# Optimization experiments

Hardware: AMD Instinct MI355X
Metric: run time of the kernel (lower is better)

## Reference

```python
import jax, jax.numpy as jnp
import numpy as np

LATENT = 1024
RED = 4            # reduce_proj
GROUPS = 16
K = 3              # kernel_size
PAD = 1
REGIONS = 36
CPG = LATENT // GROUPS   # channels per group (in and out), = 64
NEG = 0.1                # LeakyReLU slope


def l2norm(x, axis=-1):
    # faithful to lavse l2norm: x / sqrt(sum(x^2)) with no eps
    return x / jnp.sqrt(jnp.sum(x * x, axis=axis, keepdims=True))


def leaky(x):
    return jnp.where(x > 0, x, NEG * x)


def setup_inputs() -> dict:
    key = jax.random.key(0)
    ks = jax.random.split(key, 7)
    Bi, Bc, T = 128, 32, 50
    img_embed = jax.random.normal(ks[0], (Bi, REGIONS, LATENT), jnp.float32)
    cap_embed = jax.random.normal(ks[1], (Bc, T, LATENT), jnp.float32)
    lens = jax.random.randint(ks[2], (Bc,), 1, T + 1)  # word counts in [1, T]
    qdim = LATENT // RED
    s1 = 1.0 / np.sqrt(LATENT)
    red_w = jax.random.uniform(ks[3], (LATENT, qdim), jnp.float32, -s1, s1)
    red_b = jax.random.uniform(ks[4], (qdim,), jnp.float32, -s1, s1)
    nw = LATENT * CPG * K  # out_channels * (in_channels // groups) * kernel_size
    s2 = 1.0 / np.sqrt(qdim)
    proj_w = jax.random.uniform(ks[5], (qdim, nw), jnp.float32, -s2, s2)
    proj_b = jax.random.uniform(ks[6], (nw,), jnp.float32, -s2, s2)
    return dict(img_embed=img_embed, cap_embed=cap_embed, lens=lens,
                red_w=red_w, red_b=red_b, proj_w=proj_w, proj_b=proj_b)


def reference(img_embed, cap_embed, lens, red_w, red_b, proj_w, proj_b):
    Bi = img_embed.shape[0]
    Bc, T, C = cap_embed.shape
    # masked mean over the first n_words of each caption -> (Bc, C)
    mask = (jnp.arange(T)[None, :] < lens[:, None]).astype(cap_embed.dtype)
    cap_repr = jnp.sum(cap_embed * mask[:, :, None], axis=1) / lens[:, None].astype(cap_embed.dtype)
    cap_act = leaky(cap_repr)                       # 'cap' gate, (Bc, C)
    # dynamic depthwise-grouped conv weights from reduced query
    q = cap_repr @ red_w + red_b                    # (Bc, qdim)
    w = (q @ proj_w + proj_b).reshape(Bc, LATENT, CPG, K)
    w = jax.nn.softmax(w, axis=-1)                  # weightnorm='softmax' over kernel dim
    w = w.reshape(Bc, GROUPS, CPG, CPG, K)          # (Bc, g, out/g, in/g, K)
    # grouped conv1d over 36 regions, padding=1
    img = img_embed.transpose(0, 2, 1)              # (Bi, C, L)
    imgp = jnp.pad(img, ((0, 0), (0, 0), (PAD, PAD)))
    shif = jnp.stack([imgp[:, :, k:k + REGIONS] for k in range(K)], axis=-1)  # (Bi, C, L, K)
    shif = shif.reshape(Bi, GROUPS, CPG, REGIONS, K)
    out = jnp.einsum('bgilk,ngoik->nbgol', shif, w).reshape(Bc, Bi, LATENT, REGIONS)
    out = leaky(out)
    # (x * cap).mean(-1) == x.mean(-1) * cap since cap broadcasts over positions
    img_vec = l2norm(jnp.mean(out, axis=-1) * cap_act[:, None, :])  # (Bc, Bi, C)
    cap_vec = l2norm(cap_repr)                                      # (Bc, C)
    sims = jnp.einsum('nbc,nc->bn', img_vec, cap_vec)               # (Bi, Bc)
    return sims
```

## Files before the change

kernel.cpp:

```cpp
#include <hip/hip_runtime.h>
#include <math.h>

#define LATENT 1024
#define QDIM 256
#define NW 196608
#define BI 128
#define BC 32
#define TT 50
#define REGIONS 36
#define NGROUPS 16
#define CPG 64
#define NEG 0.1f

typedef __attribute__((ext_vector_type(8))) short short8;
typedef __attribute__((ext_vector_type(16))) float f32x16;

__device__ __forceinline__ float leakyf(float x){ return x > 0.f ? x : NEG * x; }

__device__ __forceinline__ unsigned short f2bf(float x){
    union { float f; unsigned int u; } v; v.f = x;
    unsigned int r = v.u + 0x7FFFu + ((v.u >> 16) & 1u);
    return (unsigned short)(r >> 16);
}

__global__ __launch_bounds__(256) void cap_mean_kernel(
    const float* __restrict__ cap_embed, const int* __restrict__ lens,
    float* __restrict__ cap_repr, float* __restrict__ cap_act,
    float* __restrict__ norm_capr)
{
    const int n = blockIdx.x;
    const int len = lens[n];
    const float invl = 1.f / (float)len;
    const int c4 = threadIdx.x;
    const float* base = cap_embed + (size_t)n * TT * LATENT + c4 * 4;
    float4 s = {0.f, 0.f, 0.f, 0.f};
    for (int t = 0; t < len; ++t) {
        const float4 v = *reinterpret_cast<const float4*>(base + (size_t)t * LATENT);
        s.x += v.x; s.y += v.y; s.z += v.z; s.w += v.w;
    }
    float4 m = {s.x * invl, s.y * invl, s.z * invl, s.w * invl};
    *reinterpret_cast<float4*>(cap_repr + n * LATENT + c4 * 4) = m;
    const float sc = 1.f / 36.f;
    float4 a = {leakyf(m.x) * sc, leakyf(m.y) * sc, leakyf(m.z) * sc, leakyf(m.w) * sc};
    *reinterpret_cast<float4*>(cap_act + n * LATENT + c4 * 4) = a;
    float ss = m.x*m.x + m.y*m.y + m.z*m.z + m.w*m.w;
    #pragma unroll
    for (int off = 32; off; off >>= 1) ss += __shfl_xor(ss, off);
    __shared__ float red4[4];
    if ((threadIdx.x & 63) == 0) red4[threadIdx.x >> 6] = ss;
    __syncthreads();
    if (threadIdx.x == 0) norm_capr[n] = sqrtf(red4[0] + red4[1] + red4[2] + red4[3]);
}

__global__ __launch_bounds__(256) void q_kernel(
    const float* __restrict__ cap_repr, const float* __restrict__ red_w,
    const float* __restrict__ red_b, unsigned short* __restrict__ qbfF)
{
    const int cg = blockIdx.x, n = blockIdx.y;
    const int col = threadIdx.x & 31, ks = threadIdx.x >> 5;
    const float* cr = cap_repr + n * LATENT;
    float p = 0.f;
    const int r0 = ks * 128;
    for (int r = r0; r < r0 + 128; ++r)
        p = fmaf(cr[r], red_w[(size_t)r * QDIM + cg * 32 + col], p);
    __shared__ float part[256];
    part[threadIdx.x] = p;
    __syncthreads();
    if (threadIdx.x < 32) {
        float s = red_b[cg * 32 + col];
        #pragma unroll
        for (int k = 0; k < 8; ++k) s += part[k * 32 + col];
        const int r = cg * 32 + col;
        const int elem = (r >> 4) * 512 + ((r >> 3) & 1) * 256 + n * 8 + (r & 7);
        qbfF[elem] = f2bf(s);
    }
}

__global__ __launch_bounds__(512, 2) void wgen10_kernel(
    const unsigned short* __restrict__ qbfF, const float* __restrict__ proj_w,
    const float* __restrict__ proj_b, unsigned short* __restrict__ Wp2F)
{
    __shared__ float L[768 * 32];
    __shared__ float pbs[768];
    const int tid = threadIdx.x;
    const int bx = blockIdx.x;
    const int colbase = bx * 768;
    const int wv = tid >> 6, lane = tid & 63;
    const int lrow = lane & 31, khalf = lane >> 5;

    for (int i = tid; i < 768; i += 512) pbs[i] = proj_b[colbase + i];

    short8 qfr[16];
    {
        const unsigned short* qp = qbfF + (size_t)lane * 8;
        #pragma unroll
        for (int s = 0; s < 16; ++s)
            qfr[s] = *reinterpret_cast<const short8*>(qp + s * 512);
    }

    const float* pw0 = proj_w + (size_t)(khalf * 8) * NW + colbase + wv * 96 + lrow;
    const float* pw1 = pw0 + 32;
    const float* pw2 = pw0 + 64;

    float a0[8], a1[8], a2[8], b0[8], b1[8], b2[8];
    #pragma unroll
    for (int j = 0; j < 8; ++j) {
        a0[j] = pw0[(size_t)j * NW];
        a1[j] = pw1[(size_t)j * NW];
        a2[j] = pw2[(size_t)j * NW];
    }

    f32x16 acc0 = {}, acc1 = {}, acc2 = {};
    #pragma unroll
    for (int s = 0; s < 16; ++s) {
        if (s < 15) {
            const size_t roff = (size_t)((s + 1) * 16) * NW;
            #pragma unroll
            for (int j = 0; j < 8; ++j) {
                b0[j] = pw0[roff + (size_t)j * NW];
                b1[j] = pw1[roff + (size_t)j * NW];
                b2[j] = pw2[roff + (size_t)j * NW];
            }
        }
        unsigned short u0[8], u1[8], u2[8];
        #pragma unroll
        for (int j = 0; j < 8; ++j) {
            u0[j] = f2bf(a0[j]); u1[j] = f2bf(a1[j]); u2[j] = f2bf(a2[j]);
        }
        acc0 = __builtin_amdgcn_mfma_f32_32x32x16_bf16(*reinterpret_cast<const short8*>(u0), qfr[s], acc0, 0, 0, 0);
        acc1 = __builtin_amdgcn_mfma_f32_32x32x16_bf16(*reinterpret_cast<const short8*>(u1), qfr[s], acc1, 0, 0, 0);
        acc2 = __builtin_amdgcn_mfma_f32_32x32x16_bf16(*reinterpret_cast<const short8*>(u2), qfr[s], acc2, 0, 0, 0);
        #pragma unroll
        for (int j = 0; j < 8; ++j) { a0[j] = b0[j]; a1[j] = b1[j]; a2[j] = b2[j]; }
    }

    __syncthreads();
    #pragma unroll
    for (int reg = 0; reg < 16; ++reg) {
        const int rit = (reg & 3) + 8 * (reg >> 2) + 4 * khalf;
        const int c = wv * 96 + rit;
        L[c * 32 + lrow]        = acc0[reg] + pbs[c];
        L[(c + 32) * 32 + lrow] = acc1[reg] + pbs[c + 32];
        L[(c + 64) * 32 + lrow] = acc2[reg] + pbs[c + 64];
    }
    __syncthreads();

    const int g = bx >> 4;
    const int obase = (bx & 15) * 4;
    for (int idx = tid; idx < 8192; idx += 512) {
        const int n = idx & 31, i = idx >> 5;
        const int c = i * 3;
        const float x0 = L[c * 32 + n], x1 = L[(c+1)*32 + n], x2 = L[(c+2)*32 + n];
        const float m = fmaxf(fmaxf(x0, x1), x2);
        const float e0 = expf(x0 - m), e1 = expf(x1 - m), e2 = expf(x2 - m);
        const float inv = 1.f / (e0 + e1 + e2);
        const int o = obase + (i >> 6);
        const int ii = i & 63;
        const int nt = o >> 5, lrow_o = o & 31;
        const int ks = ii >> 4, kh = (ii >> 3) & 1, j = ii & 7;
        const size_t base = (size_t)(n * 16 + g) * 12288
                          + (size_t)(nt * 4 + ks) * 512
                          + kh * 256 + lrow_o * 8 + j;
        Wp2F[base]        = f2bf(e0 * inv);
        Wp2F[base + 4096] = f2bf(e1 * inv);
        Wp2F[base + 8192] = f2bf(e2 * inv);
    }
}

__global__ __launch_bounds__(576, 3) void conv5_kernel(
    const float* __restrict__ img_embed, const unsigned short* __restrict__ Wp2F,
    const float* __restrict__ cap_repr, const float* __restrict__ cap_act,
    float* __restrict__ part_dot, float* __restrict__ part_ss)
{
    const int g = blockIdx.x, bt = blockIdx.y, nq = blockIdx.z;
    const int b0 = bt * 8;
    __shared__ int4 BsmV[3072];
    char* BsmRaw = (char*)BsmV;
    __shared__ float Sw[2][9][2][64];
    const int tid = threadIdx.x;
    const int wv = tid >> 6, lane = tid & 63;
    const int lrow = lane & 31, khalf = lane >> 5;
    const int ioff = khalf * 16;

    const float* imgG = img_embed + (size_t)b0 * 36 * 1024 + g * 64;
    for (int idx = tid; idx < 2304; idx += 576) {
        const int row_img = idx >> 3, ch = idx & 7;
        const int bbs = row_img / 36;
        const int l = row_img - bbs * 36;
        const float* src = imgG + (size_t)row_img * 1024 + ch * 8;
        const float4 u = *reinterpret_cast<const float4*>(src);
        const float4 v = *reinterpret_cast<const float4*>(src + 4);
        unsigned short r8[8];
        r8[0]=f2bf(u.x); r8[1]=f2bf(u.y); r8[2]=f2bf(u.z); r8[3]=f2bf(u.w);
        r8[4]=f2bf(v.x); r8[5]=f2bf(v.y); r8[6]=f2bf(v.z); r8[7]=f2bf(v.w);
        const int arow = bbs * 38 + l + 1;
        const int byte = (arow * 128 + ch * 16) ^ ((arow & 7) << 4);
        *reinterpret_cast<int4*>(BsmRaw + byte) = *reinterpret_cast<const int4*>(r8);
    }
    if (tid < 128) {
        const int rr = tid >> 3, ch = tid & 7;
        const int arow = (rr >> 1) * 38 + (rr & 1) * 37;
        const int byte = (arow * 128 + ch * 16) ^ ((arow & 7) << 4);
        int4 z; z.x = 0; z.y = 0; z.z = 0; z.w = 0;
        *reinterpret_cast<int4*>(BsmRaw + byte) = z;
    }
    __syncthreads();

    const int rg = wv * 32 + lrow;
    const int bbr = rg / 36;
    const int abase = bbr * 38 + (rg - bbr * 36);
    short8 afr[3][4];
    #pragma unroll
    for (int k = 0; k < 3; ++k)
        #pragma unroll
        for (int ks = 0; ks < 4; ++ks) {
            const int arow = abase + k;
            const int byte = (arow * 128 + ks * 32 + ioff) ^ ((arow & 7) << 4);
            afr[k][ks] = *reinterpret_cast<const short8*>(BsmRaw + byte);
        }
    const int rbase = wv * 32;
    const int bfirst = rbase / 36;
    const int bsplit = (bfirst + 1) * 36 - rbase;
    __syncthreads();

    const int n0 = nq * 16;
    int4 st0, st1, st2;
    {
        const unsigned short* WF = Wp2F + (size_t)(n0 * 16 + g) * 12288;
        st0 = *reinterpret_cast<const int4*>(WF + (size_t)tid * 8);
        st1 = *reinterpret_cast<const int4*>(WF + (size_t)(tid + 576) * 8);
        if (tid < 384) st2 = *reinterpret_cast<const int4*>(WF + (size_t)(tid + 1152) * 8);
        *reinterpret_cast<int4*>(BsmRaw + (size_t)tid * 16) = st0;
        *reinterpret_cast<int4*>(BsmRaw + (size_t)(tid + 576) * 16) = st1;
        if (tid < 384) *reinterpret_cast<int4*>(BsmRaw + (size_t)(tid + 1152) * 16) = st2;
    }
    __syncthreads();

    for (int ni = 0; ni < 16; ++ni) {
        const int n = n0 + ni;
        char* Bcur = BsmRaw + (size_t)(ni & 1) * 24576;
        char* Bnxt = BsmRaw + (size_t)((ni + 1) & 1) * 24576;

        if (ni < 15) {
            const unsigned short* WF = Wp2F + (size_t)((n + 1) * 16 + g) * 12288;
            st0 = *reinterpret_cast<const int4*>(WF + (size_t)tid * 8);
            st1 = *reinterpret_cast<const int4*>(WF + (size_t)(tid + 576) * 8);
            if (tid < 384) st2 = *reinterpret_cast<const int4*>(WF + (size_t)(tid + 1152) * 8);
        }

        f32x16 acc0 = {}, acc1 = {};
        #pragma unroll
        for (int k = 0; k < 3; ++k) {
            #pragma unroll
            for (int ks = 0; ks < 4; ++ks) {
                const char* fb = Bcur + k * 8192 + ks * 1024 + (size_t)lane * 16;
                const short8 bf0 = *reinterpret_cast<const short8*>(fb);
                const short8 bf1 = *reinterpret_cast<const short8*>(fb + 4096);
                acc0 = __builtin_amdgcn_mfma_f32_32x32x16_bf16(afr[k][ks], bf0, acc0, 0, 0, 0);
                acc1 = __builtin_amdgcn_mfma_f32_32x32x16_bf16(afr[k][ks], bf1, acc1, 0, 0, 0);
            }
        }

        if (ni < 15) {
            *reinterpret_cast<int4*>(Bnxt + (size_t)tid * 16) = st0;
            *reinterpret_cast<int4*>(Bnxt + (size_t)(tid + 576) * 16) = st1;
            if (tid < 384) *reinterpret_cast<int4*>(Bnxt + (size_t)(tid + 1152) * 16) = st2;
        }

        float s0A = 0.f, s0B = 0.f, s1A = 0.f, s1B = 0.f;
        #pragma unroll
        for (int reg = 0; reg < 16; ++reg) {
            const int rit = (reg & 3) + 8 * (reg >> 2) + 4 * khalf;
            const float v0 = leakyf(acc0[reg]);
            const float v1 = leakyf(acc1[reg]);
            if (rit >= bsplit) { s0B += v0; s1B += v1; }
            else               { s0A += v0; s1A += v1; }
        }
        s0A += __shfl_xor(s0A, 32); s0B += __shfl_xor(s0B, 32);
        s1A += __shfl_xor(s1A, 32); s1B += __shfl_xor(s1B, 32);
        const int q = ni & 1;
        if (khalf == 0) {
            Sw[q][wv][0][lrow]      = s0A;
            Sw[q][wv][0][32 + lrow] = s1A;
            if (bsplit < 32) {
                Sw[q][wv][1][lrow]      = s0B;
                Sw[q][wv][1][32 + lrow] = s1B;
            }
        }
        __syncthreads();

        if (tid < 128) {
            const int b = tid >> 4, j = tid & 15;
            const float4 ca4 = *reinterpret_cast<const float4*>(&cap_act [n * LATENT + g * CPG + j * 4]);
            const float4 cr4 = *reinterpret_cast<const float4*>(&cap_repr[n * LATENT + g * CPG + j * 4]);
            const float cav[4] = {ca4.x, ca4.y, ca4.z, ca4.w};
            const float crv[4] = {cr4.x, cr4.y, cr4.z, cr4.w};
            float d = 0.f, ss = 0.f;
            #pragma unroll
            for (int u = 0; u < 4; ++u) {
                const int o = j * 4 + u;
                const float S = (b == 0)
                    ? Sw[q][0][0][o] + Sw[q][1][0][o]
                    : Sw[q][b][1][o] + Sw[q][b + 1][0][o];
                const float tmp = S * cav[u];
                d = fmaf(tmp, crv[u], d);
                ss = fmaf(tmp, tmp, ss);
            }
            #pragma unroll
            for (int off = 1; off <= 8; off <<= 1) {
                d += __shfl_xor(d, off);
                ss += __shfl_xor(ss, off);
            }
            if (j == 0) {
                part_dot[((size_t)n * BI + b0 + b) * NGROUPS + g] = d;
                part_ss [((size_t)n * BI + b0 + b) * NGROUPS + g] = ss;
            }
        }
    }
}

__global__ __launch_bounds__(256) void final_kernel(
    const float* __restrict__ part_dot, const float* __restrict__ part_ss,
    const float* __restrict__ norm_capr, float* __restrict__ out)
{
    const int idx = blockIdx.x * 256 + threadIdx.x;
    const int n = idx & 31;
    const int b = idx >> 5;
    const size_t base = ((size_t)n * BI + b) * NGROUPS;
    float d = 0.f, s = 0.f;
    #pragma unroll
    for (int g = 0; g < NGROUPS; ++g) { d += part_dot[base + g]; s += part_ss[base + g]; }
    out[b * BC + n] = d / (sqrtf(s) * norm_capr[n]);
}

extern "C" void kernel_launch(void* const* d_in, const int* in_sizes, int n_in,
                              void* d_out, int out_size, void* d_ws, size_t ws_size,
                              hipStream_t stream) {
    const float* img_embed = (const float*)d_in[0];
    const float* cap_embed = (const float*)d_in[1];
    const int*   lens      = (const int*)  d_in[2];
    const float* red_w     = (const float*)d_in[3];
    const float* red_b     = (const float*)d_in[4];
    const float* proj_w    = (const float*)d_in[5];
    const float* proj_b    = (const float*)d_in[6];
    float* out = (float*)d_out;

    char* ws = (char*)d_ws;
    unsigned short* Wp2F   = (unsigned short*)(ws);
    float* cap_repr  = (float*)(ws + 22020096);
    float* cap_act   = (float*)(ws + 22151168);
    unsigned short* qbfF = (unsigned short*)(ws + 22282240);
    float* norm_capr = (float*)(ws + 22315008);
    float* part_dot  = (float*)(ws + 22315520);
    float* part_ss   = (float*)(ws + 22577664);

    hipLaunchKernelGGL(cap_mean_kernel, dim3(BC), dim3(256), 0, stream,
                       cap_embed, lens, cap_repr, cap_act, norm_capr);
    hipLaunchKernelGGL(q_kernel, dim3(8, BC), dim3(256), 0, stream,
                       cap_repr, red_w, red_b, qbfF);
    hipLaunchKernelGGL(wgen10_kernel, dim3(256), dim3(512), 0, stream,
                       qbfF, proj_w, proj_b, Wp2F);
    hipLaunchKernelGGL(conv5_kernel, dim3(NGROUPS, 16, 2), dim3(576), 0, stream,
                       img_embed, Wp2F, cap_repr, cap_act, part_dot, part_ss);
    hipLaunchKernelGGL(final_kernel, dim3(16), dim3(256), 0, stream,
                       part_dot, part_ss, norm_capr, out);
}
```

Baseline: 176.6 us.

## Double image rows per conv block to reuse each loaded weight tile twice

The conv kernel now handles 16 images per block instead of 8. Each wave computes two 32-row M tiles against the same double-buffered weight tile, and the image tile stays resident in a separate shared buffer. This halves how many times each weight slice is loaded from global memory and reduces the block count. In exchange, shared memory and register pressure rise, since the high tile's A fragments are reloaded from LDS inside the loop. Grid parallelism also halves, from 512 to 256 blocks.

```diff
diff --git a/kernel.cpp b/kernel.cpp
--- a/kernel.cpp
+++ b/kernel.cpp
@@ -167,23 +167,23 @@
     }
 }
 
-__global__ __launch_bounds__(576, 3) void conv5_kernel(
+__global__ __launch_bounds__(576, 3) void conv6_kernel(
     const float* __restrict__ img_embed, const unsigned short* __restrict__ Wp2F,
     const float* __restrict__ cap_repr, const float* __restrict__ cap_act,
     float* __restrict__ part_dot, float* __restrict__ part_ss)
 {
     const int g = blockIdx.x, bt = blockIdx.y, nq = blockIdx.z;
-    const int b0 = bt * 8;
-    __shared__ int4 BsmV[3072];
-    char* BsmRaw = (char*)BsmV;
-    __shared__ float Sw[2][9][2][64];
+    const int b0 = bt * 16;
+    __shared__ char Asm[16 * 38 * 128];
+    __shared__ char Bd[2][24576];
+    __shared__ float Sw[2][18][2][64];
     const int tid = threadIdx.x;
     const int wv = tid >> 6, lane = tid & 63;
     const int lrow = lane & 31, khalf = lane >> 5;
     const int ioff = khalf * 16;
 
     const float* imgG = img_embed + (size_t)b0 * 36 * 1024 + g * 64;
-    for (int idx = tid; idx < 2304; idx += 576) {
+    for (int idx = tid; idx < 4608; idx += 576) {
         const int row_img = idx >> 3, ch = idx & 7;
         const int bbs = row_img / 36;
         const int l = row_img - bbs * 36;
@@ -195,33 +195,40 @@
         r8[4]=f2bf(v.x); r8[5]=f2bf(v.y); r8[6]=f2bf(v.z); r8[7]=f2bf(v.w);
         const int arow = bbs * 38 + l + 1;
         const int byte = (arow * 128 + ch * 16) ^ ((arow & 7) << 4);
-        *reinterpret_cast<int4*>(BsmRaw + byte) = *reinterpret_cast<const int4*>(r8);
-    }
-    if (tid < 128) {
+        *reinterpret_cast<int4*>(Asm + byte) = *reinterpret_cast<const int4*>(r8);
+    }
+    if (tid < 256) {
         const int rr = tid >> 3, ch = tid & 7;
         const int arow = (rr >> 1) * 38 + (rr & 1) * 37;
         const int byte = (arow * 128 + ch * 16) ^ ((arow & 7) << 4);
         int4 z; z.x = 0; z.y = 0; z.z = 0; z.w = 0;
-        *reinterpret_cast<int4*>(BsmRaw + byte) = z;
-    }
-    __syncthreads();
-
-    const int rg = wv * 32 + lrow;
-    const int bbr = rg / 36;
-    const int abase = bbr * 38 + (rg - bbr * 36);
-    short8 afr[3][4];
+        *reinterpret_cast<int4*>(Asm + byte) = z;
+    }
+    __syncthreads();
+
+    const int rlo = wv * 64 + lrow;
+    const int blo = rlo / 36;
+    const int abase_lo = blo * 38 + (rlo - blo * 36);
+    short8 afr[12];
     #pragma unroll
     for (int k = 0; k < 3; ++k)
         #pragma unroll
         for (int ks = 0; ks < 4; ++ks) {
-            const int arow = abase + k;
+            const int arow = abase_lo + k;
             const int byte = (arow * 128 + ks * 32 + ioff) ^ ((arow & 7) << 4);
-            afr[k][ks] = *reinterpret_cast<const short8*>(BsmRaw + byte);
-        }
-    const int rbase = wv * 32;
-    const int bfirst = rbase / 36;
-    const int bsplit = (bfirst + 1) * 36 - rbase;
-    __syncthreads();
+            afr[k * 4 + ks] = *reinterpret_cast<const short8*>(Asm + byte);
+        }
+    const int rhi = wv * 64 + 32 + lrow;
+    const int bhi = rhi / 36;
+    const int abase_hi = bhi * 38 + (rhi - bhi * 36);
+
+    int bfirstT[2], bsplitT[2];
+    #pragma unroll
+    for (int mt = 0; mt < 2; ++mt) {
+        const int rbase = (2 * wv + mt) * 32;
+        bfirstT[mt] = rbase / 36;
+        bsplitT[mt] = (bfirstT[mt] + 1) * 36 - rbase;
+    }
 
     const int n0 = nq * 16;
     int4 st0, st1, st2;
@@ -230,16 +237,16 @@
         st0 = *reinterpret_cast<const int4*>(WF + (size_t)tid * 8);
         st1 = *reinterpret_cast<const int4*>(WF + (size_t)(tid + 576) * 8);
         if (tid < 384) st2 = *reinterpret_cast<const int4*>(WF + (size_t)(tid + 1152) * 8);
-        *reinterpret_cast<int4*>(BsmRaw + (size_t)tid * 16) = st0;
-        *reinterpret_cast<int4*>(BsmRaw + (size_t)(tid + 576) * 16) = st1;
-        if (tid < 384) *reinterpret_cast<int4*>(BsmRaw + (size_t)(tid + 1152) * 16) = st2;
+        *reinterpret_cast<int4*>(Bd[0] + (size_t)tid * 16) = st0;
+        *reinterpret_cast<int4*>(Bd[0] + (size_t)(tid + 576) * 16) = st1;
+        if (tid < 384) *reinterpret_cast<int4*>(Bd[0] + (size_t)(tid + 1152) * 16) = st2;
     }
     __syncthreads();
 
     for (int ni = 0; ni < 16; ++ni) {
         const int n = n0 + ni;
-        char* Bcur = BsmRaw + (size_t)(ni & 1) * 24576;
-        char* Bnxt = BsmRaw + (size_t)((ni + 1) & 1) * 24576;
+        char* Bcur = Bd[ni & 1];
+        char* Bnxt = Bd[(ni + 1) & 1];
 
         if (ni < 15) {
             const unsigned short* WF = Wp2F + (size_t)((n + 1) * 16 + g) * 12288;
@@ -248,7 +255,7 @@
             if (tid < 384) st2 = *reinterpret_cast<const int4*>(WF + (size_t)(tid + 1152) * 8);
         }
 
-        f32x16 acc0 = {}, acc1 = {};
+        f32x16 acc[2][2] = {};
         #pragma unroll
         for (int k = 0; k < 3; ++k) {
             #pragma unroll
@@ -256,8 +263,14 @@
                 const char* fb = Bcur + k * 8192 + ks * 1024 + (size_t)lane * 16;
                 const short8 bf0 = *reinterpret_cast<const short8*>(fb);
                 const short8 bf1 = *reinterpret_cast<const short8*>(fb + 4096);
-                acc0 = __builtin_amdgcn_mfma_f32_32x32x16_bf16(afr[k][ks], bf0, acc0, 0, 0, 0);
-                acc1 = __builtin_amdgcn_mfma_f32_32x32x16_bf16(afr[k][ks], bf1, acc1, 0, 0, 0);
+                const int arh = abase_hi + k;
+                const int byteH = (arh * 128 + ks * 32 + ioff) ^ ((arh & 7) << 4);
+                const short8 ah = *reinterpret_cast<const short8*>(Asm + byteH);
+                const short8 al = afr[k * 4 + ks];
+                acc[0][0] = __builtin_amdgcn_mfma_f32_32x32x16_bf16(al, bf0, acc[0][0], 0, 0, 0);
+                acc[0][1] = __builtin_amdgcn_mfma_f32_32x32x16_bf16(al, bf1, acc[0][1], 0, 0, 0);
+                acc[1][0] = __builtin_amdgcn_mfma_f32_32x32x16_bf16(ah, bf0, acc[1][0], 0, 0, 0);
+                acc[1][1] = __builtin_amdgcn_mfma_f32_32x32x16_bf16(ah, bf1, acc[1][1], 0, 0, 0);
             }
         }
 
@@ -267,41 +280,47 @@
             if (tid < 384) *reinterpret_cast<int4*>(Bnxt + (size_t)(tid + 1152) * 16) = st2;
         }
 
-        float s0A = 0.f, s0B = 0.f, s1A = 0.f, s1B = 0.f;
-        #pragma unroll
-        for (int reg = 0; reg < 16; ++reg) {
-            const int rit = (reg & 3) + 8 * (reg >> 2) + 4 * khalf;
-            const float v0 = leakyf(acc0[reg]);
-            const float v1 = leakyf(acc1[reg]);
-            if (rit >= bsplit) { s0B += v0; s1B += v1; }
-            else               { s0A += v0; s1A += v1; }
-        }
-        s0A += __shfl_xor(s0A, 32); s0B += __shfl_xor(s0B, 32);
-        s1A += __shfl_xor(s1A, 32); s1B += __shfl_xor(s1B, 32);
         const int q = ni & 1;
-        if (khalf == 0) {
-            Sw[q][wv][0][lrow]      = s0A;
-            Sw[q][wv][0][32 + lrow] = s1A;
-            if (bsplit < 32) {
-                Sw[q][wv][1][lrow]      = s0B;
-                Sw[q][wv][1][32 + lrow] = s1B;
+        #pragma unroll
+        for (int mt = 0; mt < 2; ++mt) {
+            const int bsplit = bsplitT[mt];
+            float s0A = 0.f, s0B = 0.f, s1A = 0.f, s1B = 0.f;
+            #pragma unroll
+            for (int reg = 0; reg < 16; ++reg) {
+                const int rit = (reg & 3) + 8 * (reg >> 2) + 4 * khalf;
+                const float v0 = leakyf(acc[mt][0][reg]);
+                const float v1 = leakyf(acc[mt][1][reg]);
+                if (rit >= bsplit) { s0B += v0; s1B += v1; }
+                else               { s0A += v0; s1A += v1; }
+            }
+            s0A += __shfl_xor(s0A, 32); s0B += __shfl_xor(s0B, 32);
+            s1A += __shfl_xor(s1A, 32); s1B += __shfl_xor(s1B, 32);
+            if (khalf == 0) {
+                const int t = 2 * wv + mt;
+                Sw[q][t][0][lrow]      = s0A;
+                Sw[q][t][0][32 + lrow] = s1A;
+                if (bsplit < 32) {
+                    Sw[q][t][1][lrow]      = s0B;
+                    Sw[q][t][1][32 + lrow] = s1B;
+                }
             }
         }
         __syncthreads();
 
-        if (tid < 128) {
+        if (tid < 256) {
             const int b = tid >> 4, j = tid & 15;
+            const int ta = (36 * b) >> 5;
             const float4 ca4 = *reinterpret_cast<const float4*>(&cap_act [n * LATENT + g * CPG + j * 4]);
             const float4 cr4 = *reinterpret_cast<const float4*>(&cap_repr[n * LATENT + g * CPG + j * 4]);
             const float cav[4] = {ca4.x, ca4.y, ca4.z, ca4.w};
             const float crv[4] = {cr4.x, cr4.y, cr4.z, cr4.w};
+            const int slotA = ((32 * ta) / 36 == b) ? 0 : 1;
+            const int slotB = ((32 * (ta + 1)) / 36 == b) ? 0 : 1;
             float d = 0.f, ss = 0.f;
             #pragma unroll
             for (int u = 0; u < 4; ++u) {
                 const int o = j * 4 + u;
-                const float S = (b == 0)
-                    ? Sw[q][0][0][o] + Sw[q][1][0][o]
-                    : Sw[q][b][1][o] + Sw[q][b + 1][0][o];
+                const float S = Sw[q][ta][slotA][o] + Sw[q][ta + 1][slotB][o];
                 const float tmp = S * cav[u];
                 d = fmaf(tmp, crv[u], d);
                 ss = fmaf(tmp, tmp, ss);
@@ -360,7 +379,7 @@
                        cap_repr, red_w, red_b, qbfF);
     hipLaunchKernelGGL(wgen10_kernel, dim3(256), dim3(512), 0, stream,
                        qbfF, proj_w, proj_b, Wp2F);
-    hipLaunchKernelGGL(conv5_kernel, dim3(NGROUPS, 16, 2), dim3(576), 0, stream,
+    hipLaunchKernelGGL(conv6_kernel, dim3(NGROUPS, 8, 2), dim3(576), 0, stream,
                        img_embed, Wp2F, cap_repr, cap_act, part_dot, part_ss);
     hipLaunchKernelGGL(final_kernel, dim3(16), dim3(256), 0, stream,
                        part_dot, part_ss, norm_capr, out);
```

Measured after the change: 179.4 us. About the same (+1.6%).
